# Performance work log

Hardware: AMD Instinct MI355X
Metric: run time of the kernel (lower is better)

The kernel has to match this reference:

```python
import jax, jax.numpy as jnp
from jax import lax
import numpy as np

DECAY = 0.5   # LIF membrane leak factor
VTH = 1.0     # firing threshold


def _conv(x, w, stride, pad):
    # x: [B,C,H,W], w: [O,I,kh,kw]
    return lax.conv_general_dilated(
        x, w, (stride, stride), [(pad, pad), (pad, pad)],
        dimension_numbers=('NCHW', 'OIHW', 'NCHW'))


def _convT(x, w, b, stride=2, pad=1):
    # torch ConvTranspose2d(in,out,k,stride,pad): w is [Cin,Cout,k,k]
    k = w.shape[-1]
    wf = jnp.flip(w, (-2, -1)).transpose(1, 0, 2, 3)  # -> [Cout,Cin,k,k]
    y = lax.conv_general_dilated(
        x, wf, (1, 1), [(k - 1 - pad, k - 1 - pad)] * 2,
        lhs_dilation=(stride, stride),
        dimension_numbers=('NCHW', 'OIHW', 'NCHW'))
    return y + b[None, :, None, None]


def setup_inputs() -> dict:
    key = jax.random.key(0)
    ks = jax.random.split(key, 8)
    T, B = 16, 32
    x_seq = (jax.random.uniform(ks[0], (T, B, 1, 100, 368)) < 0.1).astype(jnp.float32)

    def p(k, shape, fan_in):
        return jax.random.normal(k, shape, jnp.float32) * (1.0 / np.sqrt(fan_in))

    return {
        'x_seq': x_seq,
        'w1': p(ks[1], (16, 1, 5, 5), 25),
        'w2': p(ks[2], (32, 16, 3, 3), 16 * 9),
        'wd': p(ks[3], (64, 32, 3, 3), 32 * 9),
        'bd': jnp.zeros((64,), jnp.float32),
        'wt1': p(ks[4], (64, 32, 4, 4), 64 * 16),
        'bt1': jnp.zeros((32,), jnp.float32),
        'wt2': p(ks[5], (32, 2, 4, 4), 32 * 16),
        'bt2': jnp.zeros((2,), jnp.float32),
        'actual_batch_size': 32,
    }


def reference(x_seq, w1, w2, wd, bd, wt1, bt1, wt2, bt2, actual_batch_size):
    B = x_seq.shape[1]
    dt = x_seq.dtype
    mem1 = jnp.zeros((B, 16, 50, 184), dt)
    mem2 = jnp.zeros((B, 32, 25, 92), dt)

    def step(carry, x):
        m1, m2 = carry
        # spiking conv layer 1: leaky integrate, fire, hard reset
        m1 = m1 * DECAY + _conv(x, w1, 2, 2)
        s1 = (m1 >= VTH).astype(dt)
        m1 = m1 * (1.0 - s1)
        # spiking conv layer 2 (return_dense -> membrane kept for decoder)
        m2 = m2 * DECAY + _conv(s1, w2, 2, 1)
        s2 = (m2 >= VTH).astype(dt)
        m2 = m2 * (1.0 - s2)
        return (m1, m2), None

    (mem1, mem2), _ = lax.scan(step, (mem1, mem2), x_seq)

    # dense CNN decoder on final membrane state
    h = jax.nn.relu(_conv(mem2, wd, 1, 1) + bd[None, :, None, None])   # [B,64,25,92]
    h = jax.nn.relu(_convT(h, wt1, bt1))                               # [B,32,50,184]
    out = jax.nn.softplus(_convT(h, wt2, bt2))                         # [B,2,100,368]
    inv_tau_c_pred = out[:, 0:1]
    alpha_pred = out[:, 1:2]
    return inv_tau_c_pred, alpha_pred
```

## Files before the change

kernel.cpp:

```cpp
#include <hip/hip_runtime.h>
#include <hip/hip_bf16.h>
#include <cstddef>


#define T_STEPS 16
#define NB 32
#define H0 100
#define W0 368
#define C1 16
#define H1 50
#define W1 184
#define C2 32
#define H2 25
#define W2 92
#define CD 64
#define WPR 6
#define SITES2 2300
#define SITES1 9200

using f32x16 = __attribute__((ext_vector_type(16))) float;
using s16x8  = __attribute__((ext_vector_type(8))) short;

__device__ inline unsigned short f2bf(float f) {
    union { float f; unsigned int u; } v; v.f = f;
    unsigned int r = v.u + 0x7fffu + ((v.u >> 16) & 1u);
    return (unsigned short)(r >> 16);
}
__device__ inline float bf2f(unsigned short u) {
    union { unsigned int u; float f; } v; v.u = ((unsigned int)u) << 16;
    return v.f;
}
__device__ inline unsigned int pk2(float a, float b) {
    return (unsigned int)f2bf(a) | ((unsigned int)f2bf(b) << 16);
}
__device__ inline s16x8 ld8(const void* p) { return *reinterpret_cast<const s16x8*>(p); }

__global__ __launch_bounds__(256) void k_pack(const float* __restrict__ x,
                                              unsigned long long* __restrict__ xb) {
    long long gid = (long long)blockIdx.x * blockDim.x + threadIdx.x;
    long long widx = gid >> 6;
    int lane = (int)(gid & 63);
    const long long NWORDS = (long long)T_STEPS * NB * H0 * WPR;
    if (widx >= NWORDS) return;
    int wcol = (int)(widx % WPR);
    long long rowid = widx / WPR;
    int y = (int)(rowid % H0);
    long long tb = rowid / H0;
    int col = wcol * 64 + lane;
    float v = 0.f;
    if (col < W0) v = x[(tb * H0 + y) * W0 + col];
    unsigned long long mask = __ballot(v != 0.f);
    if (lane == 0) xb[widx] = mask;
}

__global__ __launch_bounds__(256) void k_snn1(const unsigned long long* __restrict__ xb,
                                              const float* __restrict__ w1,
                                              unsigned short* __restrict__ s1m) {
    __shared__ float sw[25 * C1];
    for (int i = threadIdx.x; i < 25 * C1; i += blockDim.x) {
        int k = i >> 4, c = i & 15;
        sw[i] = w1[c * 25 + k];
    }
    __syncthreads();

    int idx = blockIdx.x * blockDim.x + threadIdx.x;
    const int NPOS = NB * H1 * W1;
    if (idx >= NPOS) return;
    int x1 = idx % W1;
    int tmp = idx / W1;
    int y1 = tmp % H1;
    int b  = tmp / H1;

    float m1[C1];
#pragma unroll
    for (int c = 0; c < C1; ++c) m1[c] = 0.f;

    const int iy0 = 2 * y1 - 2;
    const int ix0 = 2 * x1 - 2;
    const int wi = ix0 >> 6;
    const int s  = ix0 & 63;

    for (int t = 0; t < T_STEPS; ++t) {
#pragma unroll
        for (int c = 0; c < C1; ++c) m1[c] *= 0.5f;

        const unsigned long long* xp = xb + ((size_t)(t * NB + b) * H0) * WPR;
        unsigned int bits25 = 0;
#pragma unroll
        for (int ky = 0; ky < 5; ++ky) {
            int iy = iy0 + ky;
            if (iy < 0 || iy >= H0) continue;
            const unsigned long long* row = xp + (size_t)iy * WPR;
            unsigned long long a = (wi >= 0) ? row[wi] : 0ull;
            unsigned long long bw = (wi + 1 < WPR) ? row[wi + 1] : 0ull;
            unsigned long long chunk = a >> s;
            if (s) chunk |= (bw << (64 - s));
            bits25 |= ((unsigned int)chunk & 31u) << (5 * ky);
        }
        while (bits25) {
            int k = __ffs(bits25) - 1;
            bits25 &= bits25 - 1;
            const float* wk = &sw[k * C1];
#pragma unroll
            for (int c = 0; c < C1; ++c) m1[c] += wk[c];
        }
        unsigned int mask = 0;
#pragma unroll
        for (int c = 0; c < C1; ++c) {
            if (m1[c] >= 1.0f) { mask |= (1u << c); m1[c] = 0.f; }
        }
        s1m[(size_t)t * NPOS + idx] = (unsigned short)mask;
    }
}

__global__ __launch_bounds__(256) void k_snn2(const unsigned short* __restrict__ s1m,
                                              const unsigned short* __restrict__ w2b3,
                                              unsigned short* __restrict__ mem2bf) {
    __shared__ uint4 lut[256];
    {
        int m = (int)threadIdx.x;
        unsigned int wv[4];
#pragma unroll
        for (int h = 0; h < 4; ++h) {
            unsigned int lo = (m >> (2 * h)) & 1u, hb = (m >> (2 * h + 1)) & 1u;
            wv[h] = (lo ? 0x3F80u : 0u) | (hb ? 0x3F800000u : 0u);
        }
        lut[m] = make_uint4(wv[0], wv[1], wv[2], wv[3]);
    }
    __syncthreads();

    int wave = threadIdx.x >> 6;
    int lane = threadIdx.x & 63;
    int col = lane & 31, hi = lane >> 5;
    int gsite = (blockIdx.x * 4 + wave) * 32 + col;
    int b = gsite / SITES2;
    int rest = gsite % SITES2;
    int y2 = rest / W2, x2 = rest % W2;

    int toff[9]; bool tval[9];
#pragma unroll
    for (int ky = 0; ky < 3; ++ky)
#pragma unroll
        for (int kx = 0; kx < 3; ++kx) {
            int iy = 2 * y2 + ky - 1, ix = 2 * x2 + kx - 1;
            tval[ky * 3 + kx] = iy >= 0 && iy < H1 && ix >= 0 && ix < W1;
            toff[ky * 3 + kx] = iy * W1 + ix;
        }

    const char* ab = (const char*)w2b3;
    s16x8 a0[9], a1[9], a2[9];
#pragma unroll
    for (int s = 0; s < 9; ++s) {
        int ko = (s * 16 + hi * 8) * 2;
        a0[s] = ld8(ab + (col * 144) * 2 + ko);
        a1[s] = ld8(ab + ((32 + col) * 144) * 2 + ko);
        a2[s] = ld8(ab + ((64 + col) * 144) * 2 + ko);
    }

    f32x16 acc = {};
    int hsh = hi * 8;

    for (int t = 0; t < T_STEPS; ++t) {
        const unsigned short* spk = s1m + (size_t)t * (NB * H1 * W1) + (size_t)b * (H1 * W1);
        unsigned int msk[9];
#pragma unroll
        for (int i = 0; i < 9; ++i)
            msk[i] = tval[i] ? (unsigned int)spk[toff[i]] : 0u;

#pragma unroll
        for (int e = 0; e < 16; ++e) acc[e] *= 0.5f;

#pragma unroll
        for (int s = 0; s < 9; ++s) {
            unsigned int byte = (msk[s] >> hsh) & 0xFFu;
            s16x8 bf = *reinterpret_cast<const s16x8*>(&lut[byte]);
            acc = __builtin_amdgcn_mfma_f32_32x32x16_bf16(a0[s], bf, acc, 0, 0, 0);
            acc = __builtin_amdgcn_mfma_f32_32x32x16_bf16(a1[s], bf, acc, 0, 0, 0);
            acc = __builtin_amdgcn_mfma_f32_32x32x16_bf16(a2[s], bf, acc, 0, 0, 0);
        }
#pragma unroll
        for (int e = 0; e < 16; ++e) {
            float v = acc[e];
            acc[e] = (v >= 1.0f) ? 0.f : v;
        }
    }

    char* obase = (char*)(mem2bf + (size_t)gsite * C2);
#pragma unroll
    for (int q = 0; q < 4; ++q) {
        int co = 8 * q + 4 * hi;
        uint2 u;
        u.x = pk2(acc[4 * q + 0], acc[4 * q + 1]);
        u.y = pk2(acc[4 * q + 2], acc[4 * q + 3]);
        *(uint2*)(obase + co * 2) = u;
    }
}

__global__ __launch_bounds__(256) void k_repackb(const float* __restrict__ wd,
                                                 const float* __restrict__ wt1,
                                                 const float* __restrict__ wt2,
                                                 const float* __restrict__ w2,
                                                 unsigned short* __restrict__ wdb,
                                                 unsigned short* __restrict__ wt1b,
                                                 float* __restrict__ wt2k,
                                                 unsigned short* __restrict__ w2b3) {
    int gid = blockIdx.x * blockDim.x + threadIdx.x;
    if (gid < 64 * 288) {
        int co = gid / 288, k = gid % 288;
        int tap = k >> 5, ci = k & 31;
        wdb[gid] = f2bf(wd[((size_t)co * C2 + ci) * 9 + tap]);
    } else if (gid < 64 * 288 + 4 * 32 * 256) {
        int j = gid - 64 * 288;
        int par = j >> 13, co = (j >> 8) & 31, k = j & 255;
        int tap = k >> 6, ci = k & 63;
        int ty = tap >> 1, tx = tap & 1;
        int ry = par >> 1, rx = par & 1;
        int ky = ry ? (ty ? 0 : 2) : (ty ? 3 : 1);
        int kx = rx ? (tx ? 0 : 2) : (tx ? 3 : 1);
        wt1b[j] = f2bf(wt1[(((size_t)ci * 32 + co) * 4 + ky) * 4 + kx]);
    } else if (gid < 64 * 288 + 4 * 32 * 256 + 1024) {
        int j = gid - (64 * 288 + 4 * 32 * 256);
        int par = j >> 8, tap = (j >> 6) & 3, ci = (j >> 1) & 31, co = j & 1;
        int ty = tap >> 1, tx = tap & 1;
        int ry = par >> 1, rx = par & 1;
        int ky = ry ? (ty ? 0 : 2) : (ty ? 3 : 1);
        int kx = rx ? (tx ? 0 : 2) : (tx ? 3 : 1);
        wt2k[j] = wt2[(((size_t)ci * 2 + co) * 4 + ky) * 4 + kx];
    } else if (gid < 64 * 288 + 4 * 32 * 256 + 1024 + 3 * 32 * 144) {
        int j = gid - (64 * 288 + 4 * 32 * 256 + 1024);
        int p = j / 4608, rem = j % 4608;
        int co = rem / 144, k = rem % 144;
        int tap = k / 16, ci = k % 16;
        float w = w2[((size_t)co * C1 + ci) * 9 + tap];
        unsigned short b0 = f2bf(w);
        float r1 = w - bf2f(b0);
        unsigned short b1 = f2bf(r1);
        float r2 = r1 - bf2f(b1);
        unsigned short b2 = f2bf(r2);
        w2b3[j] = (p == 0) ? b0 : (p == 1) ? b1 : b2;
    }
}

__global__ __launch_bounds__(256) void k_convd(const unsigned short* __restrict__ mem2bf,
                                               const unsigned short* __restrict__ wdb,
                                               const float* __restrict__ bd,
                                               unsigned short* __restrict__ h1bf) {
    int wave = threadIdx.x >> 6;
    int lane = threadIdx.x & 63;
    int col = lane & 31, hi = lane >> 5;
    int b = blockIdx.z;
    int n0 = (blockIdx.x * 4 + wave) * 32;
    int site = n0 + col;
    bool sval = site < SITES2;
    int sc = sval ? site : 0;
    int yy = sc / W2, xx = sc % W2;

    const char* ibase = (const char*)(mem2bf + (size_t)b * SITES2 * C2);
    int toff[9];
    bool tval[9];
#pragma unroll
    for (int ky = 0; ky < 3; ++ky)
#pragma unroll
        for (int kx = 0; kx < 3; ++kx) {
            int iy = yy + ky - 1, ix = xx + kx - 1;
            bool v = sval && iy >= 0 && iy < H2 && ix >= 0 && ix < W2;
            tval[ky * 3 + kx] = v;
            toff[ky * 3 + kx] = (iy * W2 + ix) * (C2 * 2);
        }

    const char* abase = (const char*)wdb;
    f32x16 acc0 = {}, acc1 = {};
    const s16x8 zero = {0, 0, 0, 0, 0, 0, 0, 0};
#pragma unroll
    for (int s = 0; s < 18; ++s) {
        int tap = s >> 1;
        int boff = (s & 1) * 32 + hi * 16;
        s16x8 bf = tval[tap] ? ld8(ibase + toff[tap] + boff) : zero;
        s16x8 a0 = ld8(abase + col * 576 + s * 32 + hi * 16);
        s16x8 a1 = ld8(abase + (col + 32) * 576 + s * 32 + hi * 16);
        acc0 = __builtin_amdgcn_mfma_f32_32x32x16_bf16(a0, bf, acc0, 0, 0, 0);
        acc1 = __builtin_amdgcn_mfma_f32_32x32x16_bf16(a1, bf, acc1, 0, 0, 0);
    }
    if (!sval) return;
    char* obase = (char*)(h1bf + ((size_t)b * SITES2 + site) * CD);
#pragma unroll
    for (int t = 0; t < 2; ++t) {
        const f32x16& ac = t ? acc1 : acc0;
#pragma unroll
        for (int q = 0; q < 4; ++q) {
            int co = t * 32 + 8 * q + 4 * hi;
            float v0 = fmaxf(ac[4 * q + 0] + bd[co + 0], 0.f);
            float v1 = fmaxf(ac[4 * q + 1] + bd[co + 1], 0.f);
            float v2 = fmaxf(ac[4 * q + 2] + bd[co + 2], 0.f);
            float v3 = fmaxf(ac[4 * q + 3] + bd[co + 3], 0.f);
            uint2 u; u.x = pk2(v0, v1); u.y = pk2(v2, v3);
            *(uint2*)(obase + co * 2) = u;
        }
    }
}

__global__ __launch_bounds__(256) void k_convt1(const unsigned short* __restrict__ h1bf,
                                                const unsigned short* __restrict__ wt1b,
                                                const float* __restrict__ bt1,
                                                unsigned short* __restrict__ h2bf) {
    int wave = threadIdx.x >> 6;
    int lane = threadIdx.x & 63;
    int col = lane & 31, hi = lane >> 5;
    int par = blockIdx.y;
    int ry = par >> 1, rx = par & 1;
    int b = blockIdx.z;
    int n0 = (blockIdx.x * 4 + wave) * 64;

    const char* ibase = (const char*)(h1bf + (size_t)b * SITES2 * CD);
    int toff[2][4];
    bool tval[2][4];
    int mm[2], nn[2];
    bool sv[2];
#pragma unroll
    for (int j = 0; j < 2; ++j) {
        int site = n0 + j * 32 + col;
        sv[j] = site < SITES2;
        int sc = sv[j] ? site : 0;
        int m = sc / W2, n = sc % W2;
        mm[j] = m; nn[j] = n;
        int iy1 = m + (ry ? 1 : -1);
        int ix1 = n + (rx ? 1 : -1);
        bool y1v = iy1 >= 0 && iy1 < H2;
        bool x1v = ix1 >= 0 && ix1 < W2;
#pragma unroll
        for (int t = 0; t < 4; ++t) {
            int ty = t >> 1, tx = t & 1;
            int iy = ty ? iy1 : m;
            int ix = tx ? ix1 : n;
            tval[j][t] = sv[j] && (ty ? y1v : true) && (tx ? x1v : true);
            toff[j][t] = (iy * W2 + ix) * (CD * 2);
        }
    }

    const char* abase = (const char*)(wt1b + (size_t)par * 32 * 256);
    f32x16 acc0 = {}, acc1 = {};
    const s16x8 zero = {0, 0, 0, 0, 0, 0, 0, 0};
#pragma unroll
    for (int s = 0; s < 16; ++s) {
        int tap = s >> 2;
        int boff = (s & 3) * 32 + hi * 16;
        s16x8 b0 = tval[0][tap] ? ld8(ibase + toff[0][tap] + boff) : zero;
        s16x8 b1 = tval[1][tap] ? ld8(ibase + toff[1][tap] + boff) : zero;
        s16x8 a = ld8(abase + col * 512 + s * 32 + hi * 16);
        acc0 = __builtin_amdgcn_mfma_f32_32x32x16_bf16(a, b0, acc0, 0, 0, 0);
        acc1 = __builtin_amdgcn_mfma_f32_32x32x16_bf16(a, b1, acc1, 0, 0, 0);
    }
#pragma unroll
    for (int j = 0; j < 2; ++j) {
        if (!sv[j]) continue;
        const f32x16& ac = j ? acc1 : acc0;
        int oy = 2 * mm[j] + ry, ox = 2 * nn[j] + rx;
        char* obase = (char*)(h2bf + ((size_t)b * SITES1 + (size_t)oy * W1 + ox) * C2);
#pragma unroll
        for (int q = 0; q < 4; ++q) {
            int co = 8 * q + 4 * hi;
            float v0 = fmaxf(ac[4 * q + 0] + bt1[co + 0], 0.f);
            float v1 = fmaxf(ac[4 * q + 1] + bt1[co + 1], 0.f);
            float v2 = fmaxf(ac[4 * q + 2] + bt1[co + 2], 0.f);
            float v3 = fmaxf(ac[4 * q + 3] + bt1[co + 3], 0.f);
            uint2 u; u.x = pk2(v0, v1); u.y = pk2(v2, v3);
            *(uint2*)(obase + co * 2) = u;
        }
    }
}

__global__ __launch_bounds__(256) void k_convt2(const unsigned short* __restrict__ h2bf,
                                                const float* __restrict__ wt2k,
                                                const float* __restrict__ bt2,
                                                float* __restrict__ out) {
    int i = blockIdx.x * blockDim.x + threadIdx.x;
    if (i >= SITES1) return;
    int par = blockIdx.y;
    int ry = par >> 1, rx = par & 1;
    int b = blockIdx.z;
    int m = i / W1, n = i % W1;
    int iy1 = m + (ry ? 1 : -1);
    int ix1 = n + (rx ? 1 : -1);
    bool y1v = iy1 >= 0 && iy1 < H1;
    bool x1v = ix1 >= 0 && ix1 < W1;

    float a0 = bt2[0], a1 = bt2[1];
    const unsigned short* ib = h2bf + (size_t)b * SITES1 * C2;
#pragma unroll
    for (int t = 0; t < 4; ++t) {
        int ty = t >> 1, tx = t & 1;
        if ((ty && !y1v) || (tx && !x1v)) continue;
        int iy = ty ? iy1 : m;
        int ix = tx ? ix1 : n;
        const unsigned short* p = ib + ((size_t)iy * W1 + ix) * C2;
        const float* w = wt2k + ((size_t)par * 4 + t) * 64;
#pragma unroll
        for (int g = 0; g < 4; ++g) {
            s16x8 v8 = ld8(p + g * 8);
#pragma unroll
            for (int e = 0; e < 8; ++e) {
                float v = bf2f((unsigned short)v8[e]);
                int ci = g * 8 + e;
                a0 += v * w[2 * ci];
                a1 += v * w[2 * ci + 1];
            }
        }
    }
    int oy = 2 * m + ry, ox = 2 * n + rx;
    size_t base_o = (size_t)b * (H0 * W0) + (size_t)oy * W0 + ox;
    out[base_o] = fmaxf(a0, 0.f) + log1pf(expf(-fabsf(a0)));
    out[(size_t)NB * H0 * W0 + base_o] = fmaxf(a1, 0.f) + log1pf(expf(-fabsf(a1)));
}

extern "C" void kernel_launch(void* const* d_in, const int* in_sizes, int n_in,
                              void* d_out, int out_size, void* d_ws, size_t ws_size,
                              hipStream_t stream) {
    const float* x   = (const float*)d_in[0];
    const float* w1  = (const float*)d_in[1];
    const float* w2  = (const float*)d_in[2];
    const float* wd  = (const float*)d_in[3];
    const float* bd  = (const float*)d_in[4];
    const float* wt1 = (const float*)d_in[5];
    const float* bt1 = (const float*)d_in[6];
    const float* wt2 = (const float*)d_in[7];
    const float* bt2 = (const float*)d_in[8];
    float* out = (float*)d_out;

    char* ws = (char*)d_ws;
    unsigned short* s1m    = (unsigned short*)(ws);
    unsigned short* mem2bf = (unsigned short*)(ws + 9420800);
    unsigned short* h1bf   = (unsigned short*)(ws + 14131200);
    unsigned short* h2bf   = (unsigned short*)(ws + 23552000);
    unsigned long long* xb = (unsigned long long*)(ws + 42393600);
    unsigned short* wdb    = (unsigned short*)(ws + 44851200);
    unsigned short* wt1b   = (unsigned short*)(ws + 44888064);
    float* wt2k            = (float*)(ws + 44953600);
    unsigned short* w2b3   = (unsigned short*)(ws + 44957696);

    {
        int n = 64 * 288 + 4 * 32 * 256 + 1024 + 3 * 32 * 144;
        k_repackb<<<(n + 255) / 256, 256, 0, stream>>>(wd, wt1, wt2, w2, wdb, wt1b, wt2k, w2b3);
    }
    {
        long long nthreads = (long long)T_STEPS * NB * H0 * WPR * 64;
        int blocks = (int)((nthreads + 255) / 256);
        k_pack<<<blocks, 256, 0, stream>>>(x, xb);
    }
    {
        int n = NB * H1 * W1;
        k_snn1<<<(n + 255) / 256, 256, 0, stream>>>(xb, w1, s1m);
    }
    {
        k_snn2<<<575, 256, 0, stream>>>(s1m, w2b3, mem2bf);
    }
    {
        dim3 g(18, 1, NB);
        k_convd<<<g, 256, 0, stream>>>(mem2bf, wdb, bd, h1bf);
    }
    {
        dim3 g(9, 4, NB);
        k_convt1<<<g, 256, 0, stream>>>(h1bf, wt1b, bt1, h2bf);
    }
    {
        dim3 g(36, 4, NB);
        k_convt2<<<g, 256, 0, stream>>>(h2bf, wt2k, bt2, out);
    }
}
```

Measured before the change: 207.4 us.

## Compute SNN layer-1 conv with bf16 MFMA using 3-way split weights

Replaces the per-thread sparse scatter-add over active taps in the first spiking conv with MFMA 16x16x32 bf16 matrix ops. Input spike bits are shuffled across lanes and expanded to bf16 one-hot vectors through a shared LUT. The fp32 weights are split into three bf16 parts to keep accuracy, and spike masks are assembled with cross-lane shuffles. This is meant to remove divergent, data-dependent loops and LDS reads, at the cost of dense work on a sparse input and extra shuffles.

```diff
diff --git a/kernel.cpp b/kernel.cpp
--- a/kernel.cpp
+++ b/kernel.cpp
@@ -19,6 +19,7 @@
 #define SITES1 9200
 
 using f32x16 = __attribute__((ext_vector_type(16))) float;
+using f32x4  = __attribute__((ext_vector_type(4))) float;
 using s16x8  = __attribute__((ext_vector_type(8))) short;
 
 __device__ inline unsigned short f2bf(float f) {
@@ -54,36 +55,49 @@
 }
 
 __global__ __launch_bounds__(256) void k_snn1(const unsigned long long* __restrict__ xb,
-                                              const float* __restrict__ w1,
+                                              const unsigned short* __restrict__ w1b3,
                                               unsigned short* __restrict__ s1m) {
-    __shared__ float sw[25 * C1];
-    for (int i = threadIdx.x; i < 25 * C1; i += blockDim.x) {
-        int k = i >> 4, c = i & 15;
-        sw[i] = w1[c * 25 + k];
+    __shared__ uint4 lut[256];
+    {
+        int m = (int)threadIdx.x;
+        unsigned int wv[4];
+#pragma unroll
+        for (int h = 0; h < 4; ++h) {
+            unsigned int lo = (m >> (2 * h)) & 1u, hb = (m >> (2 * h + 1)) & 1u;
+            wv[h] = (lo ? 0x3F80u : 0u) | (hb ? 0x3F800000u : 0u);
+        }
+        lut[m] = make_uint4(wv[0], wv[1], wv[2], wv[3]);
     }
     __syncthreads();
 
-    int idx = blockIdx.x * blockDim.x + threadIdx.x;
+    int wave = threadIdx.x >> 6;
+    int lane = threadIdx.x & 63;
+    int col = lane & 15;
+    int hi  = lane >> 4;
     const int NPOS = NB * H1 * W1;
-    if (idx >= NPOS) return;
-    int x1 = idx % W1;
-    int tmp = idx / W1;
-    int y1 = tmp % H1;
-    int b  = tmp / H1;
-
-    float m1[C1];
-#pragma unroll
-    for (int c = 0; c < C1; ++c) m1[c] = 0.f;
-
+    int base = (blockIdx.x * 4 + wave) * 64;
+
+    int site = base + lane;
+    int x1 = site % W1;
+    int tq = site / W1;
+    int y1 = tq % H1;
+    int b  = tq / H1;
     const int iy0 = 2 * y1 - 2;
     const int ix0 = 2 * x1 - 2;
     const int wi = ix0 >> 6;
-    const int s  = ix0 & 63;
+    const int sh = ix0 & 63;
+
+    s16x8 af0 = ld8((const char*)w1b3 + (size_t)((0 * 16 + col) * 32 + hi * 8) * 2);
+    s16x8 af1 = ld8((const char*)w1b3 + (size_t)((1 * 16 + col) * 32 + hi * 8) * 2);
+    s16x8 af2 = ld8((const char*)w1b3 + (size_t)((2 * 16 + col) * 32 + hi * 8) * 2);
+
+    f32x4 acc0 = {}, acc1 = {}, acc2 = {}, acc3 = {};
 
     for (int t = 0; t < T_STEPS; ++t) {
 #pragma unroll
-        for (int c = 0; c < C1; ++c) m1[c] *= 0.5f;
-
+        for (int e = 0; e < 4; ++e) {
+            acc0[e] *= 0.5f; acc1[e] *= 0.5f; acc2[e] *= 0.5f; acc3[e] *= 0.5f;
+        }
         const unsigned long long* xp = xb + ((size_t)(t * NB + b) * H0) * WPR;
         unsigned int bits25 = 0;
 #pragma unroll
@@ -93,23 +107,37 @@
             const unsigned long long* row = xp + (size_t)iy * WPR;
             unsigned long long a = (wi >= 0) ? row[wi] : 0ull;
             unsigned long long bw = (wi + 1 < WPR) ? row[wi + 1] : 0ull;
-            unsigned long long chunk = a >> s;
-            if (s) chunk |= (bw << (64 - s));
+            unsigned long long chunk = a >> sh;
+            if (sh) chunk |= (bw << (64 - sh));
             bits25 |= ((unsigned int)chunk & 31u) << (5 * ky);
         }
-        while (bits25) {
-            int k = __ffs(bits25) - 1;
-            bits25 &= bits25 - 1;
-            const float* wk = &sw[k * C1];
-#pragma unroll
-            for (int c = 0; c < C1; ++c) m1[c] += wk[c];
-        }
-        unsigned int mask = 0;
-#pragma unroll
-        for (int c = 0; c < C1; ++c) {
-            if (m1[c] >= 1.0f) { mask |= (1u << c); m1[c] = 0.f; }
-        }
-        s1m[(size_t)t * NPOS + idx] = (unsigned short)mask;
+#pragma unroll
+        for (int g = 0; g < 4; ++g) {
+            unsigned int sb = __shfl(bits25, g * 16 + col, 64);
+            unsigned int byte = (sb >> (hi * 8)) & 0xFFu;
+            s16x8 bf = *reinterpret_cast<const s16x8*>(&lut[byte]);
+            f32x4& ac = (g == 0) ? acc0 : (g == 1) ? acc1 : (g == 2) ? acc2 : acc3;
+            ac = __builtin_amdgcn_mfma_f32_16x16x32_bf16(af0, bf, ac, 0, 0, 0);
+            ac = __builtin_amdgcn_mfma_f32_16x16x32_bf16(af1, bf, ac, 0, 0, 0);
+            ac = __builtin_amdgcn_mfma_f32_16x16x32_bf16(af2, bf, ac, 0, 0, 0);
+        }
+#pragma unroll
+        for (int g = 0; g < 4; ++g) {
+            f32x4& ac = (g == 0) ? acc0 : (g == 1) ? acc1 : (g == 2) ? acc2 : acc3;
+            unsigned int nib = 0;
+#pragma unroll
+            for (int e = 0; e < 4; ++e) {
+                float v = ac[e];
+                bool s = (v >= 1.0f);
+                if (s) nib |= (1u << e);
+                ac[e] = s ? 0.f : v;
+            }
+            unsigned int mk = nib << (hi * 4);
+            mk |= __shfl_xor(mk, 16, 64);
+            mk |= __shfl_xor(mk, 32, 64);
+            if (lane < 16)
+                s1m[(size_t)t * NPOS + base + g * 16 + lane] = (unsigned short)mk;
+        }
     }
 }
 
@@ -200,10 +228,12 @@
                                                  const float* __restrict__ wt1,
                                                  const float* __restrict__ wt2,
                                                  const float* __restrict__ w2,
+                                                 const float* __restrict__ w1,
                                                  unsigned short* __restrict__ wdb,
                                                  unsigned short* __restrict__ wt1b,
                                                  float* __restrict__ wt2k,
-                                                 unsigned short* __restrict__ w2b3) {
+                                                 unsigned short* __restrict__ w2b3,
+                                                 unsigned short* __restrict__ w1b3) {
     int gid = blockIdx.x * blockDim.x + threadIdx.x;
     if (gid < 64 * 288) {
         int co = gid / 288, k = gid % 288;
@@ -238,6 +268,17 @@
         float r2 = r1 - bf2f(b1);
         unsigned short b2 = f2bf(r2);
         w2b3[j] = (p == 0) ? b0 : (p == 1) ? b1 : b2;
+    } else if (gid < 64 * 288 + 4 * 32 * 256 + 1024 + 3 * 32 * 144 + 3 * 16 * 32) {
+        int j = gid - (64 * 288 + 4 * 32 * 256 + 1024 + 3 * 32 * 144);
+        int p = j / 512, rem = j % 512;
+        int co = rem / 32, k = rem % 32;
+        float w = (k < 25) ? w1[co * 25 + k] : 0.f;
+        unsigned short b0 = f2bf(w);
+        float r1 = w - bf2f(b0);
+        unsigned short b1 = f2bf(r1);
+        float r2 = r1 - bf2f(b1);
+        unsigned short b2 = f2bf(r2);
+        w1b3[j] = (p == 0) ? b0 : (p == 1) ? b1 : b2;
     }
 }
 
@@ -436,10 +477,12 @@
     unsigned short* wt1b   = (unsigned short*)(ws + 44888064);
     float* wt2k            = (float*)(ws + 44953600);
     unsigned short* w2b3   = (unsigned short*)(ws + 44957696);
-
-    {
-        int n = 64 * 288 + 4 * 32 * 256 + 1024 + 3 * 32 * 144;
-        k_repackb<<<(n + 255) / 256, 256, 0, stream>>>(wd, wt1, wt2, w2, wdb, wt1b, wt2k, w2b3);
+    unsigned short* w1b3   = (unsigned short*)(ws + 44985344);
+
+    {
+        int n = 64 * 288 + 4 * 32 * 256 + 1024 + 3 * 32 * 144 + 3 * 16 * 32;
+        k_repackb<<<(n + 255) / 256, 256, 0, stream>>>(wd, wt1, wt2, w2, w1,
+                                                       wdb, wt1b, wt2k, w2b3, w1b3);
     }
     {
         long long nthreads = (long long)T_STEPS * NB * H0 * WPR * 64;
@@ -447,8 +490,7 @@
         k_pack<<<blocks, 256, 0, stream>>>(x, xb);
     }
     {
-        int n = NB * H1 * W1;
-        k_snn1<<<(n + 255) / 256, 256, 0, stream>>>(xb, w1, s1m);
+        k_snn1<<<1150, 256, 0, stream>>>(xb, w1b3, s1m);
     }
     {
         k_snn2<<<575, 256, 0, stream>>>(s1m, w2b3, mem2bf);
```

Result: faster. 200.2 us (-3.5%).
